# Performance work log

Measured on AMD Instinct MI355X. Metric: run time of the kernel, lower is better.

## Reference

```python
import jax, jax.numpy as jnp
import numpy as np
from jax import lax

RES = 2048
MAX_VAL = 1.0
COST_SCALE = 0.01
N_ITERS = 10
BOUNDARY_FRAC = 0.02  # sparse scattered Dirichlet cells, realistic for a planner occupancy grid


def _neighbor_sum(V):
    # replicate-pad (zero-Neumann at the outer border), 4-point stencil sum
    Vp = jnp.pad(V, 1, mode='edge')
    return Vp[:-2, 1:-1] + Vp[2:, 1:-1] + Vp[1:-1, :-2] + Vp[1:-1, 2:]


def setup_inputs() -> dict:
    key = jax.random.key(0)
    k1, k2, k3, k4 = jax.random.split(key, 4)
    x = jax.random.uniform(k1, (RES, RES), jnp.float32)
    # sparse boundary/obstacle cells (boundary_types > 0 means Dirichlet cell)
    boundary_types = (jax.random.uniform(k2, (RES, RES)) < BOUNDARY_FRAC).astype(jnp.int32)
    boundary_conditions = jax.random.uniform(k3, (RES, RES), jnp.float32)
    # learnable cost field, initialized around cost_scale (some negatives so ReLU matters)
    C = COST_SCALE + COST_SCALE * jax.random.normal(k4, (RES, RES), jnp.float32)
    return {'x': x, 'C': C, 'boundary_types': boundary_types,
            'boundary_conditions': boundary_conditions}


def reference(x, C, boundary_types, boundary_conditions):
    mask = boundary_types > 0
    # inject boundary conditions into the initial potential (x[obj_inds] = bc[obj_inds])
    V = jnp.where(mask, boundary_conditions, x)
    C_pos = jax.nn.relu(C)
    denom = 4.0 + C_pos  # screened Laplace: (4 + C) V = sum(neighbors)

    def step(V, _):
        V_new = _neighbor_sum(V) / denom
        V_new = jnp.where(mask, boundary_conditions, V_new)
        return V_new, None

    V, _ = lax.scan(step, V, None, length=N_ITERS)

    out = jnp.where(V >= MAX_VAL, 0.95 * MAX_VAL, V)
    out = jnp.where(mask, boundary_conditions, out)
    return out, C_pos
```

## Files before the change

kernel.cpp:

```cpp
#include <hip/hip_runtime.h>


#define RES    2048
#define XHALO  12
#define YHALO  10
#define DIMX   128
#define DIMY   56
#define OUTX   (DIMX - 2*XHALO)
#define OUTY   (DIMY - 2*YHALO)
#define NBX    ((RES + OUTX - 1) / OUTX)
#define NBY    ((RES + OUTY - 1) / OUTY)
#define NWG    (NBX*NBY)
#define NITER  10

__global__ __launch_bounds__(256, 4)
void laplace10_fused(const float* __restrict__ Xin,
                     const float* __restrict__ Cin,
                     const float* __restrict__ BTf,
                     const float* __restrict__ BCin,
                     float* __restrict__ OUT,
                     float* __restrict__ CPOS) {
  __shared__ __align__(16) float V[DIMY][DIMX];

  const int t  = threadIdx.x;
  const int q  = t & 31;
  const int ty = t >> 5;
  const int x0 = q * 4;
  const int y0 = ty * 7;

  int wg = (int)blockIdx.x;
  {
    const int qq = NWG / 8, rr = NWG % 8;
    const int xcd = wg % 8, off = wg / 8;
    wg = (xcd < rr ? xcd * (qq + 1) : rr * (qq + 1) + (xcd - rr) * qq) + off;
  }
  const int bx  = wg % NBX, by = wg / NBX;
  const int tx0 = bx * OUTX - XHALO;
  const int ty0 = by * OUTY - YHALO;
  const int gx0 = tx0 + x0;

  const bool xfull = (gx0 >= 0) && (gx0 + 4 <= RES);
  const int  xcl   = (gx0 < 0) ? 0 : (RES - 1);
  const bool xin   = (x0 >= XHALO) && (x0 < XHALO + OUTX) && xfull;

  auto load4 = [&](const float* __restrict__ g, int row) -> float4 {
    if (xfull) return *(const float4*)(g + (size_t)row * RES + gx0);
    const float v = g[(size_t)row * RES + xcl];
    return make_float4(v, v, v, v);
  };

  const bool lq0 = (gx0 + 0 <= 0);
  const bool lq1 = (gx0 + 1 <= 0);
  const bool lq2 = (gx0 + 2 <= 0);
  const bool lq3 = (gx0 + 3 <= 0);
  const bool rq0 = (gx0 + 0 >= RES - 1);
  const bool rq1 = (gx0 + 1 >= RES - 1);
  const bool rq2 = (gx0 + 2 >= RES - 1);
  const bool rq3 = (gx0 + 3 >= RES - 1);

  unsigned mb = 0u;
  float4 Bq[7], Rq[7];
#pragma unroll
  for (int i = 0; i < 7; ++i) {
    const int gr  = ty0 + y0 + i;
    const int gyc = gr < 0 ? 0 : (gr > RES - 1 ? RES - 1 : gr);
    const float4 mv = load4(BTf, gyc);
    const float4 bv = load4(BCin, gyc);
    const unsigned m0 = (__float_as_uint(mv.x) != 0u);
    const unsigned m1 = (__float_as_uint(mv.y) != 0u);
    const unsigned m2 = (__float_as_uint(mv.z) != 0u);
    const unsigned m3 = (__float_as_uint(mv.w) != 0u);
    mb |= (m0 | (m1 << 1) | (m2 << 2) | (m3 << 3)) << (4 * i);
    Bq[i].x = m0 ? bv.x : 0.0f;
    Bq[i].y = m1 ? bv.y : 0.0f;
    Bq[i].z = m2 ? bv.z : 0.0f;
    Bq[i].w = m3 ? bv.w : 0.0f;
  }
#pragma unroll
  for (int i = 0; i < 7; ++i) {
    const int gr  = ty0 + y0 + i;
    const int gyc = gr < 0 ? 0 : (gr > RES - 1 ? RES - 1 : gr);
    const float4 c = load4(Cin, gyc);
    float4 cp;
    cp.x = c.x > 0.0f ? c.x : 0.0f;
    cp.y = c.y > 0.0f ? c.y : 0.0f;
    cp.z = c.z > 0.0f ? c.z : 0.0f;
    cp.w = c.w > 0.0f ? c.w : 0.0f;
    Rq[i].x = (mb >> (4 * i + 0) & 1u) ? 0.0f : 1.0f / (4.0f + cp.x);
    Rq[i].y = (mb >> (4 * i + 1) & 1u) ? 0.0f : 1.0f / (4.0f + cp.y);
    Rq[i].z = (mb >> (4 * i + 2) & 1u) ? 0.0f : 1.0f / (4.0f + cp.z);
    Rq[i].w = (mb >> (4 * i + 3) & 1u) ? 0.0f : 1.0f / (4.0f + cp.w);
    const int yy = y0 + i;
    if (xin && yy >= YHALO && yy < YHALO + OUTY && gr >= 0 && gr < RES) {
      *(float4*)(CPOS + (size_t)gr * RES + gx0) = cp;
    }
  }
#pragma unroll
  for (int i = 0; i < 7; ++i) {
    const int gr  = ty0 + y0 + i;
    const int gyc = gr < 0 ? 0 : (gr > RES - 1 ? RES - 1 : gr);
    const float4 xv = load4(Xin, gyc);
    float4 v0;
    v0.x = (mb >> (4 * i + 0) & 1u) ? Bq[i].x : xv.x;
    v0.y = (mb >> (4 * i + 1) & 1u) ? Bq[i].y : xv.y;
    v0.z = (mb >> (4 * i + 2) & 1u) ? Bq[i].z : xv.z;
    v0.w = (mb >> (4 * i + 3) & 1u) ? Bq[i].w : xv.w;
    *(float4*)(&V[y0 + i][x0]) = v0;
  }
  __syncthreads();

  auto compute_ns = [&](float4* ns) {
    const int ym1 = (y0 == 0) ? 0 : y0 - 1;
    float4 ra = *(const float4*)(&V[ym1][x0]);
    float4 rb = *(const float4*)(&V[y0][x0]);
#pragma unroll
    for (int i = 0; i < 7; ++i) {
      const int yy = y0 + i;
      const int yp = (yy >= DIMY - 1) ? (DIMY - 1) : (yy + 1);
      const float4 rc = *(const float4*)(&V[yp][x0]);
      const float lf = __shfl(rb.w, (t + 63) & 63);
      const float rt = __shfl(rb.x, (t + 1) & 63);
      const int g = ty0 + yy;
      const float4 vm = rb;
      const float4 va = (g <= 0) ? vm : ra;
      const float4 vb = (g >= RES - 1) ? vm : rc;
      float4 n;
      n.x = va.x + vb.x + (lq0 ? vm.x : lf)   + (rq0 ? vm.x : vm.y);
      n.y = va.y + vb.y + (lq1 ? vm.y : vm.x) + (rq1 ? vm.y : vm.z);
      n.z = va.z + vb.z + (lq2 ? vm.z : vm.y) + (rq2 ? vm.z : vm.w);
      n.w = va.w + vb.w + (lq3 ? vm.w : vm.z) + (rq3 ? vm.w : rt);
      ns[i] = n;
      ra = rb; rb = rc;
    }
  };

#pragma unroll 1
  for (int it = 1; it < NITER; ++it) {
    float4 ns[7];
    compute_ns(ns);
    __syncthreads();
#pragma unroll
    for (int i = 0; i < 7; ++i) {
      const int yy = y0 + i;
      if (yy >= it && yy < DIMY - it) {
        float4 nv;
        nv.x = fmaf(ns[i].x, Rq[i].x, Bq[i].x);
        nv.y = fmaf(ns[i].y, Rq[i].y, Bq[i].y);
        nv.z = fmaf(ns[i].z, Rq[i].z, Bq[i].z);
        nv.w = fmaf(ns[i].w, Rq[i].w, Bq[i].w);
        *(float4*)(&V[yy][x0]) = nv;
      }
    }
    __syncthreads();
  }

  {
    float4 ns[7];
    compute_ns(ns);
#pragma unroll
    for (int i = 0; i < 7; ++i) {
      const int yy = y0 + i;
      if (xin && yy >= YHALO && yy < YHALO + OUTY) {
        const int g = ty0 + yy;
        if (g < RES) {
          float4 nv;
          nv.x = fmaf(ns[i].x, Rq[i].x, Bq[i].x);
          nv.y = fmaf(ns[i].y, Rq[i].y, Bq[i].y);
          nv.z = fmaf(ns[i].z, Rq[i].z, Bq[i].z);
          nv.w = fmaf(ns[i].w, Rq[i].w, Bq[i].w);
          float4 o;
          o.x = (nv.x >= 1.0f) ? 0.95f : nv.x;
          o.y = (nv.y >= 1.0f) ? 0.95f : nv.y;
          o.z = (nv.z >= 1.0f) ? 0.95f : nv.z;
          o.w = (nv.w >= 1.0f) ? 0.95f : nv.w;
          *(float4*)(OUT + (size_t)g * RES + gx0) = o;
        }
      }
    }
  }
}

extern "C" void kernel_launch(void* const* d_in, const int* in_sizes, int n_in,
                              void* d_out, int out_size, void* d_ws, size_t ws_size,
                              hipStream_t stream) {
  const float* Xin  = (const float*)d_in[0];
  const float* Cin  = (const float*)d_in[1];
  const float* BTf  = (const float*)d_in[2];
  const float* BCin = (const float*)d_in[3];
  float* OUT  = (float*)d_out;
  float* CPOS = OUT + (size_t)RES * RES;

  hipLaunchKernelGGL(laplace10_fused, dim3(NWG), dim3(256), 0, stream,
                     Xin, Cin, BTf, BCin, OUT, CPOS);
}
```

Measured before the change: 153.8 us.

## Double-buffer shared tile, keep rows in registers, use 512-thread blocks

Grows the tile to 64 rows and the block to 512 threads, so each thread owns 4 rows instead of 7. Each thread keeps its current rows in registers and reads only the top and bottom halo rows from shared memory. Ping-pong shared buffers remove one of the two barriers per iteration. The cost is twice the shared memory per block, which may lower occupancy, and the wider halo overhead changes with the new tile height.

Measured after the change: 131.1 us. 14.7% less time.

```diff
diff --git a/kernel.cpp b/kernel.cpp
--- a/kernel.cpp
+++ b/kernel.cpp
@@ -5,7 +5,7 @@
 #define XHALO  12
 #define YHALO  10
 #define DIMX   128
-#define DIMY   56
+#define DIMY   64
 #define OUTX   (DIMX - 2*XHALO)
 #define OUTY   (DIMY - 2*YHALO)
 #define NBX    ((RES + OUTX - 1) / OUTX)
@@ -13,20 +13,20 @@
 #define NWG    (NBX*NBY)
 #define NITER  10
 
-__global__ __launch_bounds__(256, 4)
+__global__ __launch_bounds__(512, 4)
 void laplace10_fused(const float* __restrict__ Xin,
                      const float* __restrict__ Cin,
                      const float* __restrict__ BTf,
                      const float* __restrict__ BCin,
                      float* __restrict__ OUT,
                      float* __restrict__ CPOS) {
-  __shared__ __align__(16) float V[DIMY][DIMX];
+  __shared__ __align__(16) float V[2][DIMY][DIMX];
 
   const int t  = threadIdx.x;
   const int q  = t & 31;
   const int ty = t >> 5;
   const int x0 = q * 4;
-  const int y0 = ty * 7;
+  const int y0 = ty * 4;
 
   int wg = (int)blockIdx.x;
   {
@@ -41,7 +41,7 @@
 
   const bool xfull = (gx0 >= 0) && (gx0 + 4 <= RES);
   const int  xcl   = (gx0 < 0) ? 0 : (RES - 1);
-  const bool xin   = (x0 >= XHALO) && (x0 < XHALO + OUTX) && xfull;
+  const bool xin   = xfull && (x0 >= XHALO) && (x0 < XHALO + OUTX);
 
   auto load4 = [&](const float* __restrict__ g, int row) -> float4 {
     if (xfull) return *(const float4*)(g + (size_t)row * RES + gx0);
@@ -59,125 +59,112 @@
   const bool rq3 = (gx0 + 3 >= RES - 1);
 
   unsigned mb = 0u;
-  float4 Bq[7], Rq[7];
+  float4 Bq[4], Rq[4], cur[4];
 #pragma unroll
-  for (int i = 0; i < 7; ++i) {
-    const int gr  = ty0 + y0 + i;
-    const int gyc = gr < 0 ? 0 : (gr > RES - 1 ? RES - 1 : gr);
-    const float4 mv = load4(BTf, gyc);
-    const float4 bv = load4(BCin, gyc);
+  for (int j = 0; j < 4; ++j) {
+    const int yy = y0 + j;
+    const int g  = ty0 + yy;
+    const int gc = g < 0 ? 0 : (g > RES - 1 ? RES - 1 : g);
+    const float4 mv = load4(BTf, gc);
+    const float4 bv = load4(BCin, gc);
+    const float4 cv = load4(Cin, gc);
+    const float4 xv = load4(Xin, gc);
     const unsigned m0 = (__float_as_uint(mv.x) != 0u);
     const unsigned m1 = (__float_as_uint(mv.y) != 0u);
     const unsigned m2 = (__float_as_uint(mv.z) != 0u);
     const unsigned m3 = (__float_as_uint(mv.w) != 0u);
-    mb |= (m0 | (m1 << 1) | (m2 << 2) | (m3 << 3)) << (4 * i);
-    Bq[i].x = m0 ? bv.x : 0.0f;
-    Bq[i].y = m1 ? bv.y : 0.0f;
-    Bq[i].z = m2 ? bv.z : 0.0f;
-    Bq[i].w = m3 ? bv.w : 0.0f;
-  }
-#pragma unroll
-  for (int i = 0; i < 7; ++i) {
-    const int gr  = ty0 + y0 + i;
-    const int gyc = gr < 0 ? 0 : (gr > RES - 1 ? RES - 1 : gr);
-    const float4 c = load4(Cin, gyc);
+    mb |= (m0 | (m1 << 1) | (m2 << 2) | (m3 << 3)) << (4 * j);
+    float4 B;
+    B.x = m0 ? bv.x : 0.0f;  B.y = m1 ? bv.y : 0.0f;
+    B.z = m2 ? bv.z : 0.0f;  B.w = m3 ? bv.w : 0.0f;
+    Bq[j] = B;
     float4 cp;
-    cp.x = c.x > 0.0f ? c.x : 0.0f;
-    cp.y = c.y > 0.0f ? c.y : 0.0f;
-    cp.z = c.z > 0.0f ? c.z : 0.0f;
-    cp.w = c.w > 0.0f ? c.w : 0.0f;
-    Rq[i].x = (mb >> (4 * i + 0) & 1u) ? 0.0f : 1.0f / (4.0f + cp.x);
-    Rq[i].y = (mb >> (4 * i + 1) & 1u) ? 0.0f : 1.0f / (4.0f + cp.y);
-    Rq[i].z = (mb >> (4 * i + 2) & 1u) ? 0.0f : 1.0f / (4.0f + cp.z);
-    Rq[i].w = (mb >> (4 * i + 3) & 1u) ? 0.0f : 1.0f / (4.0f + cp.w);
-    const int yy = y0 + i;
-    if (xin && yy >= YHALO && yy < YHALO + OUTY && gr >= 0 && gr < RES) {
-      *(float4*)(CPOS + (size_t)gr * RES + gx0) = cp;
+    cp.x = cv.x > 0.0f ? cv.x : 0.0f;
+    cp.y = cv.y > 0.0f ? cv.y : 0.0f;
+    cp.z = cv.z > 0.0f ? cv.z : 0.0f;
+    cp.w = cv.w > 0.0f ? cv.w : 0.0f;
+    float4 R;
+    R.x = m0 ? 0.0f : 1.0f / (4.0f + cp.x);
+    R.y = m1 ? 0.0f : 1.0f / (4.0f + cp.y);
+    R.z = m2 ? 0.0f : 1.0f / (4.0f + cp.z);
+    R.w = m3 ? 0.0f : 1.0f / (4.0f + cp.w);
+    Rq[j] = R;
+    float4 v0;
+    v0.x = m0 ? B.x : xv.x;  v0.y = m1 ? B.y : xv.y;
+    v0.z = m2 ? B.z : xv.z;  v0.w = m3 ? B.w : xv.w;
+    cur[j] = v0;
+    *(float4*)(&V[0][yy][x0]) = v0;
+    if (xin && yy >= YHALO && yy < YHALO + OUTY && g < RES) {
+      *(float4*)(CPOS + (size_t)g * RES + gx0) = cp;
     }
-  }
-#pragma unroll
-  for (int i = 0; i < 7; ++i) {
-    const int gr  = ty0 + y0 + i;
-    const int gyc = gr < 0 ? 0 : (gr > RES - 1 ? RES - 1 : gr);
-    const float4 xv = load4(Xin, gyc);
-    float4 v0;
-    v0.x = (mb >> (4 * i + 0) & 1u) ? Bq[i].x : xv.x;
-    v0.y = (mb >> (4 * i + 1) & 1u) ? Bq[i].y : xv.y;
-    v0.z = (mb >> (4 * i + 2) & 1u) ? Bq[i].z : xv.z;
-    v0.w = (mb >> (4 * i + 3) & 1u) ? Bq[i].w : xv.w;
-    *(float4*)(&V[y0 + i][x0]) = v0;
   }
   __syncthreads();
 
-  auto compute_ns = [&](float4* ns) {
-    const int ym1 = (y0 == 0) ? 0 : y0 - 1;
-    float4 ra = *(const float4*)(&V[ym1][x0]);
-    float4 rb = *(const float4*)(&V[y0][x0]);
-#pragma unroll
-    for (int i = 0; i < 7; ++i) {
-      const int yy = y0 + i;
-      const int yp = (yy >= DIMY - 1) ? (DIMY - 1) : (yy + 1);
-      const float4 rc = *(const float4*)(&V[yp][x0]);
-      const float lf = __shfl(rb.w, (t + 63) & 63);
-      const float rt = __shfl(rb.x, (t + 1) & 63);
-      const int g = ty0 + yy;
-      const float4 vm = rb;
-      const float4 va = (g <= 0) ? vm : ra;
-      const float4 vb = (g >= RES - 1) ? vm : rc;
-      float4 n;
-      n.x = va.x + vb.x + (lq0 ? vm.x : lf)   + (rq0 ? vm.x : vm.y);
-      n.y = va.y + vb.y + (lq1 ? vm.y : vm.x) + (rq1 ? vm.y : vm.z);
-      n.z = va.z + vb.z + (lq2 ? vm.z : vm.y) + (rq2 ? vm.z : vm.w);
-      n.w = va.w + vb.w + (lq3 ? vm.w : vm.z) + (rq3 ? vm.w : rt);
-      ns[i] = n;
-      ra = rb; rb = rc;
+  const int ytop = (ty == 0)  ? 0        : y0 - 1;
+  const int ybot = (ty == 15) ? DIMY - 1 : y0 + 4;
+
+  #define ROW_STEP(J, VP, VM, VN, NV)                                          \
+    {                                                                          \
+      const int g_ = ty0 + y0 + (J);                                           \
+      const float lf = __shfl((VM).w, (t + 63) & 63);                          \
+      const float rt = __shfl((VM).x, (t + 1) & 63);                           \
+      const float4 va = (g_ <= 0)       ? (VM) : (VP);                         \
+      const float4 vb = (g_ >= RES - 1) ? (VM) : (VN);                         \
+      const float n0 = va.x + vb.x + (lq0 ? (VM).x : lf)     + (rq0 ? (VM).x : (VM).y); \
+      const float n1 = va.y + vb.y + (lq1 ? (VM).y : (VM).x) + (rq1 ? (VM).y : (VM).z); \
+      const float n2 = va.z + vb.z + (lq2 ? (VM).z : (VM).y) + (rq2 ? (VM).z : (VM).w); \
+      const float n3 = va.w + vb.w + (lq3 ? (VM).w : (VM).z) + (rq3 ? (VM).w : rt);     \
+      (NV).x = fmaf(n0, Rq[J].x, Bq[J].x);                                     \
+      (NV).y = fmaf(n1, Rq[J].y, Bq[J].y);                                     \
+      (NV).z = fmaf(n2, Rq[J].z, Bq[J].z);                                     \
+      (NV).w = fmaf(n3, Rq[J].w, Bq[J].w);                                     \
     }
-  };
 
 #pragma unroll 1
   for (int it = 1; it < NITER; ++it) {
-    float4 ns[7];
-    compute_ns(ns);
-    __syncthreads();
-#pragma unroll
-    for (int i = 0; i < 7; ++i) {
-      const int yy = y0 + i;
-      if (yy >= it && yy < DIMY - it) {
-        float4 nv;
-        nv.x = fmaf(ns[i].x, Rq[i].x, Bq[i].x);
-        nv.y = fmaf(ns[i].y, Rq[i].y, Bq[i].y);
-        nv.z = fmaf(ns[i].z, Rq[i].z, Bq[i].z);
-        nv.w = fmaf(ns[i].w, Rq[i].w, Bq[i].w);
-        *(float4*)(&V[yy][x0]) = nv;
-      }
-    }
+    const float* const src = &V[(it + 1) & 1][0][0];
+    float* const dst       = &V[it & 1][0][0];
+    const float4 top = *(const float4*)(src + ytop * DIMX + x0);
+    const float4 bot = *(const float4*)(src + ybot * DIMX + x0);
+    float4 n0v, n1v, n2v, n3v;
+    ROW_STEP(0, top,    cur[0], cur[1], n0v);
+    ROW_STEP(1, cur[0], cur[1], cur[2], n1v);
+    ROW_STEP(2, cur[1], cur[2], cur[3], n2v);
+    ROW_STEP(3, cur[2], cur[3], bot,    n3v);
+    cur[0] = n0v; cur[1] = n1v; cur[2] = n2v; cur[3] = n3v;
+    *(float4*)(dst + (y0 + 0) * DIMX + x0) = n0v;
+    *(float4*)(dst + (y0 + 1) * DIMX + x0) = n1v;
+    *(float4*)(dst + (y0 + 2) * DIMX + x0) = n2v;
+    *(float4*)(dst + (y0 + 3) * DIMX + x0) = n3v;
     __syncthreads();
   }
 
   {
-    float4 ns[7];
-    compute_ns(ns);
+    const float* const src = &V[1][0][0];
+    const float4 top = *(const float4*)(src + ytop * DIMX + x0);
+    const float4 bot = *(const float4*)(src + ybot * DIMX + x0);
+    float4 n0v, n1v, n2v, n3v;
+    ROW_STEP(0, top,    cur[0], cur[1], n0v);
+    ROW_STEP(1, cur[0], cur[1], cur[2], n1v);
+    ROW_STEP(2, cur[1], cur[2], cur[3], n2v);
+    ROW_STEP(3, cur[2], cur[3], bot,    n3v);
+    cur[0] = n0v; cur[1] = n1v; cur[2] = n2v; cur[3] = n3v;
 #pragma unroll
-    for (int i = 0; i < 7; ++i) {
-      const int yy = y0 + i;
-      if (xin && yy >= YHALO && yy < YHALO + OUTY) {
-        const int g = ty0 + yy;
-        if (g < RES) {
-          float4 nv;
-          nv.x = fmaf(ns[i].x, Rq[i].x, Bq[i].x);
-          nv.y = fmaf(ns[i].y, Rq[i].y, Bq[i].y);
-          nv.z = fmaf(ns[i].z, Rq[i].z, Bq[i].z);
-          nv.w = fmaf(ns[i].w, Rq[i].w, Bq[i].w);
-          float4 o;
-          o.x = (nv.x >= 1.0f) ? 0.95f : nv.x;
-          o.y = (nv.y >= 1.0f) ? 0.95f : nv.y;
-          o.z = (nv.z >= 1.0f) ? 0.95f : nv.z;
-          o.w = (nv.w >= 1.0f) ? 0.95f : nv.w;
-          *(float4*)(OUT + (size_t)g * RES + gx0) = o;
-        }
+    for (int j = 0; j < 4; ++j) {
+      const int yy = y0 + j;
+      const int g  = ty0 + yy;
+      if (xin && yy >= YHALO && yy < YHALO + OUTY && g < RES) {
+        const float4 nv = cur[j];
+        float4 o;
+        o.x = (nv.x >= 1.0f) ? 0.95f : nv.x;
+        o.y = (nv.y >= 1.0f) ? 0.95f : nv.y;
+        o.z = (nv.z >= 1.0f) ? 0.95f : nv.z;
+        o.w = (nv.w >= 1.0f) ? 0.95f : nv.w;
+        *(float4*)(OUT + (size_t)g * RES + gx0) = o;
       }
     }
   }
+  #undef ROW_STEP
 }
 
 extern "C" void kernel_launch(void* const* d_in, const int* in_sizes, int n_in,
@@ -190,6 +177,6 @@
   float* OUT  = (float*)d_out;
   float* CPOS = OUT + (size_t)RES * RES;
 
-  hipLaunchKernelGGL(laplace10_fused, dim3(NWG), dim3(256), 0, stream,
+  hipLaunchKernelGGL(laplace10_fused, dim3(NWG), dim3(512), 0, stream,
                      Xin, Cin, BTf, BCin, OUT, CPOS);
 }
```
